# Kernel tuning notes

Hardware: AMD Instinct MI355X
Metric: run time of the kernel (lower is better)

## Reference

```python
import jax, jax.numpy as jnp
from jax import lax
import numpy as np

B, T, F = 256, 256, 40
H, A, HORIZON = 256, 64, 60
D_SP = 192


def setup_inputs() -> dict:
    key = jax.random.key(0)
    ks = jax.random.split(key, 16)
    s = 0.05  # weight scale to keep activations stable
    return {
        'x': jax.random.normal(ks[0], (B, T, F), jnp.float32),
        'W_sp': jax.random.normal(ks[1], (F, D_SP), jnp.float32) * s,
        'b_sp': jnp.zeros((D_SP,), jnp.float32),
        'Wx_ef': jax.random.normal(ks[2], (D_SP, 4 * H), jnp.float32) * s,
        'Wh_ef': jax.random.normal(ks[3], (H, 4 * H), jnp.float32) * s,
        'b_ef': jnp.zeros((4 * H,), jnp.float32),
        'Wx_eb': jax.random.normal(ks[4], (D_SP, 4 * H), jnp.float32) * s,
        'Wh_eb': jax.random.normal(ks[5], (H, 4 * H), jnp.float32) * s,
        'b_eb': jnp.zeros((4 * H,), jnp.float32),
        'We': jax.random.normal(ks[6], (2 * H, A), jnp.float32) * s,
        'Wd': jax.random.normal(ks[7], (H, A), jnp.float32) * s,
        'v': jax.random.normal(ks[8], (A,), jnp.float32) * s,
        'Wx_d': jax.random.normal(ks[9], (1 + 2 * H, 4 * H), jnp.float32) * s,
        'Wh_d': jax.random.normal(ks[10], (H, 4 * H), jnp.float32) * s,
        'b_d': jnp.zeros((4 * H,), jnp.float32),
        'W_ih': jax.random.normal(ks[11], (2 * H, H), jnp.float32) * s,
        'b_ih': jnp.zeros((H,), jnp.float32),
        'W_ic': jax.random.normal(ks[12], (2 * H, H), jnp.float32) * s,
        'b_ic': jnp.zeros((H,), jnp.float32),
        'Wo': jax.random.normal(ks[13], (H, 1), jnp.float32) * s,
        'bo': jnp.zeros((1,), jnp.float32),
    }


def _lstm_cell(x_t, h, c, Wx, Wh, b):
    g = x_t @ Wx + h @ Wh + b
    i, f, gg, o = jnp.split(g, 4, axis=-1)  # torch gate order i,f,g,o
    c = jax.nn.sigmoid(f) * c + jax.nn.sigmoid(i) * jnp.tanh(gg)
    h = jax.nn.sigmoid(o) * jnp.tanh(c)
    return h, c


def _lstm_scan(xs_tbd, Wx, Wh, b):
    # xs_tbd: [T, B, D] -> hs [T, B, H]
    h0 = jnp.zeros((xs_tbd.shape[1], Wh.shape[0]), xs_tbd.dtype)
    c0 = jnp.zeros_like(h0)
    def step(carry, x_t):
        h, c = carry
        h, c = _lstm_cell(x_t, h, c, Wx, Wh, b)
        return (h, c), h
    _, hs = lax.scan(step, (h0, c0), xs_tbd)
    return hs


def reference(x, W_sp, b_sp, Wx_ef, Wh_ef, b_ef, Wx_eb, Wh_eb, b_eb,
              We, Wd, v, Wx_d, Wh_d, b_d, W_ih, b_ih, W_ic, b_ic, Wo, bo):
    # spatial encoder (stand-in for DeepLOBEncoder): [B,T,F] -> [B,T,192]
    h_spatial = x @ W_sp + b_sp
    xs = jnp.swapaxes(h_spatial, 0, 1)          # [T, B, 192]
    hs_f = _lstm_scan(xs, Wx_ef, Wh_ef, b_ef)    # [T, B, H]
    hs_b = _lstm_scan(xs[::-1], Wx_eb, Wh_eb, b_eb)[::-1]
    enc_out = jnp.swapaxes(jnp.concatenate([hs_f, hs_b], axis=-1), 0, 1)  # [B,T,2H]

    enc_mean = enc_out.mean(axis=1)
    dec_h = jnp.tanh(enc_mean @ W_ih + b_ih)     # [B, H]
    dec_c = jnp.tanh(enc_mean @ W_ic + b_ic)

    enc_proj = enc_out @ We                      # [B, T, A] precomputed (same math)
    prev_y = ((x[:, -1, 0] + x[:, -1, 2]) / 2.0)[:, None]  # ask_idx=0, bid_idx=2

    def dec_step(carry, _):
        h, c, py = carry
        e = jnp.tanh(enc_proj + (h @ Wd)[:, None, :])        # [B,T,A]
        scores = e @ v                                        # [B,T]
        w = jax.nn.softmax(scores, axis=1)
        context = jnp.einsum('bt,bth->bh', w, enc_out)        # [B,2H]
        dec_in = jnp.concatenate([py, context], axis=1)       # [B,1+2H]
        h, c = _lstm_cell(dec_in, h, c, Wx_d, Wh_d, b_d)
        y = h @ Wo + bo                                       # [B,1]
        return (h, c, lax.stop_gradient(y)), y[:, 0]

    _, ys = lax.scan(dec_step, (dec_h, dec_c, prev_y), None, length=HORIZON)
    return jnp.swapaxes(ys, 0, 1)  # [B, horizon]
```

## Files before the change

kernel.cpp:

```cpp
#include <hip/hip_runtime.h>
#include <cmath>

#define B_ 256
#define T_ 256
#define F_ 40
#define H_ 256
#define A_ 64
#define HOR_ 60
#define DSP_ 192
#define ENC_NBLK 128
#define GRP_SZ 16
#define WSTR 456

typedef unsigned short u16;
typedef unsigned int u32;
typedef __attribute__((ext_vector_type(8))) short bf16x8;
typedef __attribute__((ext_vector_type(4))) float f32x4;
typedef __attribute__((ext_vector_type(8))) u32 u32x8;
typedef __attribute__((ext_vector_type(4))) u32 u32x4;

__device__ __forceinline__ float sigm(float x){ return 1.f/(1.f+expf(-x)); }

__device__ __forceinline__ u16 f2bf(float x){
  u32 u = __float_as_uint(x);
  u32 r = (u + 0x7FFFu + ((u>>16)&1u)) >> 16;
  return (u16)r;
}
__device__ __forceinline__ float bf2f(u16 h){ return __uint_as_float(((u32)h)<<16); }
__device__ __forceinline__ u32 packsplit(float x){
  u16 hi = f2bf(x);
  u16 lo = f2bf(x - bf2f(hi));
  return (u32)hi | ((u32)lo<<16);
}
__device__ __forceinline__ float unpack2f(u32 v){
  return __uint_as_float(v<<16) + __uint_as_float(v & 0xFFFF0000u);
}

__device__ __forceinline__ float wred_sum(float v){
  #pragma unroll
  for (int o=32;o>0;o>>=1) v += __shfl_xor(v,o);
  return v;
}
__device__ __forceinline__ float wred_max(float v){
  #pragma unroll
  for (int o=32;o>0;o>>=1) v = fmaxf(v,__shfl_xor(v,o));
  return v;
}

__global__ void conv_w(const float* __restrict__ Wx, const float* __restrict__ Wh,
                       u16* __restrict__ hi, u16* __restrict__ lo,
                       int KX, int Ktot, int N){
  int idx = blockIdx.x*256 + threadIdx.x;
  if (idx >= N*Ktot) return;
  int n = idx / Ktot, k = idx - n*Ktot;
  float w = (k < KX) ? Wx[(size_t)k*N + n] : Wh[(size_t)(k-KX)*N + n];
  u16 h = f2bf(w);
  hi[idx] = h;
  lo[idx] = f2bf(w - bf2f(h));
}

__global__ __launch_bounds__(192) void spatial_proj(
    const float* __restrict__ x, const float* __restrict__ W, const float* __restrict__ bsp,
    u32* __restrict__ hsp32){
  __shared__ float Ws[40][192];
  __shared__ float xr[40];
  int t = blockIdx.x, tid = threadIdx.x;
  for (int i = tid; i < 40*192; i += 192){ int k = i/192, c = i-k*192; Ws[k][c] = W[i]; }
  float bb = bsp[tid];
  __syncthreads();
  for (int b=0; b<B_; b++){
    if (tid < 40) xr[tid] = x[((size_t)b*T_ + t)*F_ + tid];
    __syncthreads();
    float acc = bb;
    #pragma unroll
    for (int k=0;k<40;k++) acc += xr[k]*Ws[k][tid];
    hsp32[((size_t)t*B_ + b)*DSP_ + tid] = packsplit(acc);
    __syncthreads();
  }
}

__global__ __launch_bounds__(256) void enc_scan(
    const u32* __restrict__ hsp32,
    const u16* __restrict__ W_hi, const u16* __restrict__ W_lo,
    const float* __restrict__ b_ef, const float* __restrict__ b_eb,
    u32* __restrict__ hbuf, u32* __restrict__ eo32, int* __restrict__ bar)
{
  extern __shared__ u16 smem[];
  u16* Whi = smem;
  u16* Wlo = smem + 4*16*WSTR;
  const int bid = blockIdx.x;
  const int grp = bid & 7;
  const int nt  = bid >> 3;
  const int dir = grp >> 2;
  const int m0  = (grp & 3) * 64;
  const int u0  = nt * 16;
  const int tid = threadIdx.x;
  const int wave = tid >> 6, lane = tid & 63;
  const int lrow = lane & 15, kblk = lane >> 4;
  const int koff = kblk * 8;
  {
    const size_t wbase = ((size_t)dir*1024 + u0) * 448;
    for (int idx = tid; idx < 4*16*448; idx += 256){
      int g = idx / (16*448);
      int r = idx - g*(16*448);
      int j = r / 448;
      int k = r - j*448;
      size_t go = wbase + ((size_t)g*256 + j)*448 + k;
      Whi[(g*16 + j)*WSTR + k] = W_hi[go];
      Wlo[(g*16 + j)*WSTR + k] = W_lo[go];
    }
  }
  const float* bias = dir ? b_eb : b_ef;
  float bg4[4];
  #pragma unroll
  for (int g=0; g<4; g++) bg4[g] = bias[g*H_ + u0 + lrow];
  __syncthreads();

  const int mrow = m0 + wave*16;
  const int arow = mrow + lrow;
  u32* hP0 = hbuf + (size_t)dir*(B_*H_);
  u32* hP1 = hbuf + (size_t)(2+dir)*(B_*H_);
  int* gbar = bar + grp*T_;
  float c_reg[4] = {0.f,0.f,0.f,0.f};

  for (int s=0; s<T_; s++){
    const int t = dir ? (T_-1-s) : s;
    f32x4 acc[4] = {};
    const u32* abase = hsp32 + ((size_t)t*B_ + arow)*DSP_;
    #pragma unroll
    for (int ks=0; ks<6; ks++){
      int kb = ks*32 + koff;
      u32x8 la = *(const u32x8*)(abase + kb);
      bf16x8 ah, al;
      #pragma unroll
      for (int j=0;j<8;j++){ ah[j]=(short)(la[j]&0xFFFFu); al[j]=(short)(la[j]>>16); }
      #pragma unroll
      for (int g=0; g<4; g++){
        bf16x8 bh = *(const bf16x8*)(Whi + (g*16+lrow)*WSTR + kb);
        bf16x8 bl = *(const bf16x8*)(Wlo + (g*16+lrow)*WSTR + kb);
        acc[g] = __builtin_amdgcn_mfma_f32_16x16x32_bf16(ah, bh, acc[g], 0,0,0);
        acc[g] = __builtin_amdgcn_mfma_f32_16x16x32_bf16(ah, bl, acc[g], 0,0,0);
        acc[g] = __builtin_amdgcn_mfma_f32_16x16x32_bf16(al, bh, acc[g], 0,0,0);
      }
    }
    if (s > 0){
      if (tid == 0){
        while (__hip_atomic_load(&gbar[s-1], __ATOMIC_ACQUIRE, __HIP_MEMORY_SCOPE_AGENT) < GRP_SZ)
          __builtin_amdgcn_s_sleep(1);
      }
      __syncthreads();
    }
    const u32* hin = (s & 1) ? hP1 : hP0;
    u32* hout      = (s & 1) ? hP0 : hP1;
    const u32* hbase = hin + (size_t)arow*H_;
    #pragma unroll
    for (int ks=0; ks<8; ks++){
      int kb = ks*32 + koff;
      u32x8 la = *(const u32x8*)(hbase + kb);
      bf16x8 ah, al;
      #pragma unroll
      for (int j=0;j<8;j++){ ah[j]=(short)(la[j]&0xFFFFu); al[j]=(short)(la[j]>>16); }
      #pragma unroll
      for (int g=0; g<4; g++){
        bf16x8 bh = *(const bf16x8*)(Whi + (g*16+lrow)*WSTR + 192 + kb);
        bf16x8 bl = *(const bf16x8*)(Wlo + (g*16+lrow)*WSTR + 192 + kb);
        acc[g] = __builtin_amdgcn_mfma_f32_16x16x32_bf16(ah, bh, acc[g], 0,0,0);
        acc[g] = __builtin_amdgcn_mfma_f32_16x16x32_bf16(ah, bl, acc[g], 0,0,0);
        acc[g] = __builtin_amdgcn_mfma_f32_16x16x32_bf16(al, bh, acc[g], 0,0,0);
      }
    }
    #pragma unroll
    for (int r=0; r<4; r++){
      int brow = mrow + kblk*4 + r;
      float gi = acc[0][r] + bg4[0];
      float gf = acc[1][r] + bg4[1];
      float gg = acc[2][r] + bg4[2];
      float go = acc[3][r] + bg4[3];
      float cn = sigm(gf)*c_reg[r] + sigm(gi)*tanhf(gg);
      float hn = sigm(go)*tanhf(cn);
      c_reg[r] = cn;
      u32 hp = packsplit(hn);
      hout[(size_t)brow*H_ + u0 + lrow] = hp;
      eo32[((size_t)brow*T_ + t)*512 + dir*H_ + u0 + lrow] = hp;
    }
    if (s == T_-1) break;
    __syncthreads();
    if (tid == 0)
      __hip_atomic_fetch_add(&gbar[s], 1, __ATOMIC_RELEASE, __HIP_MEMORY_SCOPE_AGENT);
  }
}

__global__ __launch_bounds__(512) void attn_step(
    const u32* __restrict__ eo32, const float* __restrict__ ep,
    const float* __restrict__ Wd, const float* __restrict__ v,
    const float* __restrict__ Wo, const float* __restrict__ bo,
    const float* __restrict__ h_dec, u32* __restrict__ Ad32,
    float* __restrict__ py, float* __restrict__ out, int s)
{
  __shared__ float sh_h[256], sh_hwd[64], sh_v[64], sh_sc[256], sh_w[256];
  __shared__ float red8[8][64];
  __shared__ float sh_red[4], sh_red2[4];
  __shared__ float redc[8][512];
  const int b = blockIdx.x, tid = threadIdx.x;
  const int wave = tid >> 6, lane = tid & 63;
  if (tid < 256) sh_h[tid] = h_dec[b*H_ + tid];
  if (tid >= 448) sh_v[tid-448] = v[tid-448];
  __syncthreads();
  if (s > 0) {
    if (tid < 256){
      float p = sh_h[tid] * Wo[tid];
      p = wred_sum(p);
      if ((tid & 63) == 0) sh_red[tid>>6] = p;
    }
    __syncthreads();
    if (tid == 0){
      float y = sh_red[0]+sh_red[1]+sh_red[2]+sh_red[3] + bo[0];
      out[b*HOR_ + (s-1)] = y;
      py[b] = y;
    }
  }
  {
    float ssum = 0.f;
    for (int j=wave*32; j<wave*32+32; j++) ssum += sh_h[j]*Wd[(size_t)j*A_ + lane];
    red8[wave][lane] = ssum;
    __syncthreads();
    if (tid < 64){
      float a = 0.f;
      #pragma unroll
      for (int q=0;q<8;q++) a += red8[q][tid];
      sh_hwd[tid] = a;
    }
  }
  __syncthreads();
  {
    int t = tid >> 1, aa = tid & 1;
    const float4* ep4 = (const float4*)(ep + ((size_t)(b*T_+t))*A_ + aa*32);
    float partial = 0.f;
    #pragma unroll
    for (int q=0;q<8;q++){
      float4 e4 = ep4[q];
      int a0 = aa*32 + q*4;
      partial += tanhf(e4.x + sh_hwd[a0+0]) * sh_v[a0+0];
      partial += tanhf(e4.y + sh_hwd[a0+1]) * sh_v[a0+1];
      partial += tanhf(e4.z + sh_hwd[a0+2]) * sh_v[a0+2];
      partial += tanhf(e4.w + sh_hwd[a0+3]) * sh_v[a0+3];
    }
    partial += __shfl_xor(partial, 1);
    if (aa == 0) sh_sc[t] = partial;
  }
  __syncthreads();
  if (tid < 256){
    float sc = sh_sc[tid];
    float m = wred_max(sc);
    if ((tid&63)==0) sh_red[tid>>6] = m;
    __syncthreads();
    m = fmaxf(fmaxf(sh_red[0],sh_red[1]), fmaxf(sh_red[2],sh_red[3]));
    float e = expf(sc - m);
    float su = wred_sum(e);
    if ((tid&63)==0) sh_red2[tid>>6] = su;
    __syncthreads();
    su = (sh_red2[0]+sh_red2[1])+(sh_red2[2]+sh_red2[3]);
    sh_w[tid] = e / su;
  } else { __syncthreads(); __syncthreads(); }
  __syncthreads();
  {
    float cacc[8] = {};
    const u32* eo = eo32 + (size_t)b*T_*512 + lane*8;
    #pragma unroll 8
    for (int tt=0; tt<32; tt++){
      int t = wave*32 + tt;
      float wgt = sh_w[t];
      u32x4 e0 = *(const u32x4*)(eo + (size_t)t*512);
      u32x4 e1 = *(const u32x4*)(eo + (size_t)t*512 + 4);
      #pragma unroll
      for (int j=0;j<4;j++){
        cacc[j]   += wgt * unpack2f(e0[j]);
        cacc[4+j] += wgt * unpack2f(e1[j]);
      }
    }
    #pragma unroll
    for (int j=0;j<8;j++) redc[wave][lane*8+j] = cacc[j];
  }
  __syncthreads();
  if (tid < 256){
    float c0 = 0.f, c1 = 0.f;
    #pragma unroll
    for (int q=0;q<8;q++){ c0 += redc[q][tid]; c1 += redc[q][256+tid]; }
    Ad32[(size_t)b*768 + tid]       = packsplit(c0);
    Ad32[(size_t)b*768 + 256 + tid] = packsplit(c1);
  }
}

__global__ __launch_bounds__(128) void dec_step_mfma(
    const u32* __restrict__ Ad32,
    const u16* __restrict__ W_hi, const u16* __restrict__ W_lo,
    const float* __restrict__ b_d, const float* __restrict__ Wx_d,
    const float* __restrict__ py,
    float* __restrict__ c_dec, float* __restrict__ h_dec,
    u32* __restrict__ AdW)
{
  const int u0 = blockIdx.x * 16;
  const int tid = threadIdx.x;
  const int wave = tid >> 6, lane = tid & 63;
  const int lrow = lane & 15, kblk = lane >> 4;
  const int u = u0 + lrow;
  const int mbase = blockIdx.y * 32 + wave * 16;
  const int koff = kblk * 8;
  size_t wro[4];
  #pragma unroll
  for (int g=0; g<4; g++) wro[g] = (size_t)(g*H_ + u) * 768;
  f32x4 acc[4] = {};
  const u32* abase = Ad32 + (size_t)(mbase + lrow)*768;
  for (int ks=0; ks<24; ks++){
    int kb = ks*32 + koff;
    u32x8 ld = *(const u32x8*)(abase + kb);
    bf16x8 ah, al;
    #pragma unroll
    for (int j=0;j<8;j++){ ah[j] = (short)(ld[j] & 0xFFFFu); al[j] = (short)(ld[j] >> 16); }
    #pragma unroll
    for (int g=0; g<4; g++){
      bf16x8 bh = *(const bf16x8*)(W_hi + wro[g] + kb);
      bf16x8 bl = *(const bf16x8*)(W_lo + wro[g] + kb);
      acc[g] = __builtin_amdgcn_mfma_f32_16x16x32_bf16(ah, bh, acc[g], 0,0,0);
      acc[g] = __builtin_amdgcn_mfma_f32_16x16x32_bf16(ah, bl, acc[g], 0,0,0);
      acc[g] = __builtin_amdgcn_mfma_f32_16x16x32_bf16(al, bh, acc[g], 0,0,0);
    }
  }
  float bg4[4], w0g[4];
  #pragma unroll
  for (int g=0;g<4;g++){ bg4[g] = b_d[g*H_ + u]; w0g[g] = Wx_d[g*H_ + u]; }
  #pragma unroll
  for (int r=0; r<4; r++){
    int bb = mbase + kblk*4 + r;
    float pyb = py[bb];
    float gi = acc[0][r] + bg4[0] + pyb*w0g[0];
    float gf = acc[1][r] + bg4[1] + pyb*w0g[1];
    float gg = acc[2][r] + bg4[2] + pyb*w0g[2];
    float go = acc[3][r] + bg4[3] + pyb*w0g[3];
    size_t ci = (size_t)bb*H_ + u;
    float cn = sigm(gf)*c_dec[ci] + sigm(gi)*tanhf(gg);
    float hn = sigm(go)*tanhf(cn);
    c_dec[ci] = cn;
    h_dec[ci] = hn;
    AdW[(size_t)bb*768 + 512 + u] = packsplit(hn);
  }
}

__global__ __launch_bounds__(256) void gemm_ep(
    const u32* __restrict__ eo32, const u16* __restrict__ Wet_hi, const u16* __restrict__ Wet_lo,
    float* __restrict__ ep)
{
  const int tid = threadIdx.x, wave = tid>>6, lane = tid&63;
  const int lrow = lane&15, kblk = lane>>4, koff = kblk*8;
  const size_t arow = (size_t)blockIdx.x*64 + wave*16 + lrow;
  f32x4 acc[4] = {};
  size_t wro[4];
  #pragma unroll
  for (int nf=0; nf<4; nf++) wro[nf] = (size_t)(nf*16 + lrow)*512;
  for (int ks=0; ks<16; ks++){
    int kb = ks*32 + koff;
    u32x8 ld = *(const u32x8*)(eo32 + arow*512 + kb);
    bf16x8 ah, al;
    #pragma unroll
    for (int j=0;j<8;j++){ ah[j] = (short)(ld[j] & 0xFFFFu); al[j] = (short)(ld[j] >> 16); }
    #pragma unroll
    for (int nf=0; nf<4; nf++){
      bf16x8 bh = *(const bf16x8*)(Wet_hi + wro[nf] + kb);
      bf16x8 bl = *(const bf16x8*)(Wet_lo + wro[nf] + kb);
      acc[nf] = __builtin_amdgcn_mfma_f32_16x16x32_bf16(ah, bh, acc[nf], 0,0,0);
      acc[nf] = __builtin_amdgcn_mfma_f32_16x16x32_bf16(ah, bl, acc[nf], 0,0,0);
      acc[nf] = __builtin_amdgcn_mfma_f32_16x16x32_bf16(al, bh, acc[nf], 0,0,0);
    }
  }
  #pragma unroll
  for (int nf=0; nf<4; nf++)
    #pragma unroll
    for (int r=0; r<4; r++){
      size_t orow = (size_t)blockIdx.x*64 + wave*16 + kblk*4 + r;
      ep[orow*64 + nf*16 + lrow] = acc[nf][r];
    }
}

__global__ __launch_bounds__(256) void sgemm_bias(
    const float* __restrict__ A, const float* __restrict__ W,
    const float* __restrict__ bias, float* __restrict__ C,
    int M, int N, int K, int act)
{
  __shared__ float As[64][17];
  __shared__ float Ws[16][64];
  int tid = threadIdx.x;
  int tr = tid >> 4, tc = tid & 15;
  int row0 = blockIdx.y * 64, col0 = blockIdx.x * 64;
  float acc[4][4] = {};
  for (int k0 = 0; k0 < K; k0 += 16) {
    for (int i = tid; i < 64*16; i += 256) {
      int r = i >> 4, kk = i & 15;
      int gr = row0 + r, gk = k0 + kk;
      As[r][kk] = (gr < M && gk < K) ? A[(size_t)gr*K + gk] : 0.f;
    }
    for (int i = tid; i < 16*64; i += 256) {
      int r = i >> 6, c = i & 63;
      int gk = k0 + r, gc = col0 + c;
      Ws[r][c] = (gk < K && gc < N) ? W[(size_t)gk*N + gc] : 0.f;
    }
    __syncthreads();
    #pragma unroll
    for (int kk=0;kk<16;kk++){
      float a0 = As[tr*4+0][kk], a1 = As[tr*4+1][kk];
      float a2v = As[tr*4+2][kk], a3 = As[tr*4+3][kk];
      float4 b4 = *(const float4*)&Ws[kk][tc*4];
      acc[0][0]+=a0*b4.x; acc[0][1]+=a0*b4.y; acc[0][2]+=a0*b4.z; acc[0][3]+=a0*b4.w;
      acc[1][0]+=a1*b4.x; acc[1][1]+=a1*b4.y; acc[1][2]+=a1*b4.z; acc[1][3]+=a1*b4.w;
      acc[2][0]+=a2v*b4.x; acc[2][1]+=a2v*b4.y; acc[2][2]+=a2v*b4.z; acc[2][3]+=a2v*b4.w;
      acc[3][0]+=a3*b4.x; acc[3][1]+=a3*b4.y; acc[3][2]+=a3*b4.z; acc[3][3]+=a3*b4.w;
    }
    __syncthreads();
  }
  #pragma unroll
  for (int i=0;i<4;i++){
    int r = row0 + tr*4 + i; if (r >= M) continue;
    #pragma unroll
    for (int j=0;j<4;j++){
      int c = col0 + tc*4 + j; if (c >= N) continue;
      float vv = acc[i][j] + (bias ? bias[c] : 0.f);
      if (act == 1) vv = tanhf(vv);
      C[(size_t)r*N + c] = vv;
    }
  }
}

__global__ __launch_bounds__(256) void final_y(const float* __restrict__ h_dec,
    const float* __restrict__ Wo, const float* __restrict__ bo, float* __restrict__ out){
  __shared__ float sh[4];
  int b = blockIdx.x, tid = threadIdx.x;
  float p = h_dec[b*H_+tid]*Wo[tid];
  p = wred_sum(p);
  if ((tid&63)==0) sh[tid>>6]=p;
  __syncthreads();
  if (tid==0) out[b*HOR_ + HOR_-1] = sh[0]+sh[1]+sh[2]+sh[3] + bo[0];
}

__global__ __launch_bounds__(256) void enc_mean_k(const u32* __restrict__ eo32,
                                                  float* __restrict__ em){
  __shared__ float redc[4][512];
  int b = blockIdx.x, tid = threadIdx.x;
  int wave = tid >> 6, lane = tid & 63;
  float cacc[8] = {};
  const u32* eo = eo32 + (size_t)b*T_*512 + lane*8;
  #pragma unroll 8
  for (int tt=0; tt<64; tt++){
    int t = wave*64 + tt;
    u32x4 e0 = *(const u32x4*)(eo + (size_t)t*512);
    u32x4 e1 = *(const u32x4*)(eo + (size_t)t*512 + 4);
    #pragma unroll
    for (int j=0;j<4;j++){ cacc[j] += unpack2f(e0[j]); cacc[4+j] += unpack2f(e1[j]); }
  }
  #pragma unroll
  for (int j=0;j<8;j++) redc[wave][lane*8+j] = cacc[j];
  __syncthreads();
  em[(size_t)b*512 + tid]       = (redc[0][tid]+redc[1][tid]+redc[2][tid]+redc[3][tid])*(1.f/T_);
  em[(size_t)b*512 + 256 + tid] = (redc[0][256+tid]+redc[1][256+tid]+redc[2][256+tid]+redc[3][256+tid])*(1.f/T_);
}

__global__ void pack_hd(const float* __restrict__ hd, u32* __restrict__ Ad32){
  int i = blockIdx.x*256 + threadIdx.x;
  int b = i >> 8, u = i & 255;
  Ad32[(size_t)b*768 + 512 + u] = packsplit(hd[i]);
}

__global__ void py_init(const float* __restrict__ x, float* __restrict__ py){
  int b = blockIdx.x*256 + threadIdx.x;
  if (b < B_)
    py[b] = (x[(size_t)b*T_*F_ + 255*F_ + 0] +
             x[(size_t)b*T_*F_ + 255*F_ + 2]) * 0.5f;
}

extern "C" void kernel_launch(void* const* d_in, const int* in_sizes, int n_in,
                              void* d_out, int out_size, void* d_ws, size_t ws_size,
                              hipStream_t stream)
{
  const float* x    = (const float*)d_in[0];
  const float* W_sp = (const float*)d_in[1];
  const float* b_sp = (const float*)d_in[2];
  const float* Wx_ef= (const float*)d_in[3];
  const float* Wh_ef= (const float*)d_in[4];
  const float* b_ef = (const float*)d_in[5];
  const float* Wx_eb= (const float*)d_in[6];
  const float* Wh_eb= (const float*)d_in[7];
  const float* b_eb = (const float*)d_in[8];
  const float* We   = (const float*)d_in[9];
  const float* Wd   = (const float*)d_in[10];
  const float* v    = (const float*)d_in[11];
  const float* Wx_d = (const float*)d_in[12];
  const float* Wh_d = (const float*)d_in[13];
  const float* b_d  = (const float*)d_in[14];
  const float* W_ih = (const float*)d_in[15];
  const float* b_ih = (const float*)d_in[16];
  const float* W_ic = (const float*)d_in[17];
  const float* b_ic = (const float*)d_in[18];
  const float* Wo   = (const float*)d_in[19];
  const float* bo   = (const float*)d_in[20];
  float* out = (float*)d_out;

  char* base = (char*)d_ws;
  auto alloc = [&](size_t bytes)->char*{
    char* p = base; base += (bytes + 255) & ~(size_t)255; return p;
  };
  u16* Wenc_hi = (u16*)alloc((size_t)2*1024*448*2);
  u16* Wenc_lo = (u16*)alloc((size_t)2*1024*448*2);
  u16* Wdec_hi = (u16*)alloc((size_t)1024*768*2);
  u16* Wdec_lo = (u16*)alloc((size_t)1024*768*2);
  u16* Wet_hi  = (u16*)alloc((size_t)64*512*2);
  u16* Wet_lo  = (u16*)alloc((size_t)64*512*2);
  u32* hsp32   = (u32*)alloc((size_t)T_*B_*DSP_*4);
  u32* hbuf    = (u32*)alloc((size_t)2*2*B_*H_*4);
  u32* eo32    = (u32*)alloc((size_t)B_*T_*512*4);
  float* em    = (float*)alloc((size_t)B_*512*4);
  float* ep    = (float*)alloc((size_t)B_*T_*64*4);
  float* hd    = (float*)alloc((size_t)B_*H_*4);
  float* cd    = (float*)alloc((size_t)B_*H_*4);
  u32* Ad32    = (u32*)alloc((size_t)B_*768*4);
  float* pyb   = (float*)alloc((size_t)B_*4);
  int* bar     = (int*)alloc((size_t)8*T_*4);
  if ((size_t)(base - (char*)d_ws) > ws_size) return;

  conv_w<<<dim3(1792),256,0,stream>>>(Wx_ef, Wh_ef, Wenc_hi, Wenc_lo, DSP_, 448, 1024);
  conv_w<<<dim3(1792),256,0,stream>>>(Wx_eb, Wh_eb, Wenc_hi+458752, Wenc_lo+458752, DSP_, 448, 1024);
  conv_w<<<dim3(3072),256,0,stream>>>(Wx_d+1024, Wh_d, Wdec_hi, Wdec_lo, 512, 768, 1024);
  conv_w<<<dim3(128),256,0,stream>>>(We, We, Wet_hi, Wet_lo, 512, 512, 64);

  spatial_proj<<<dim3(256),192,0,stream>>>(x, W_sp, b_sp, hsp32);

  hipMemsetAsync(hbuf, 0, (size_t)2*B_*H_*4, stream);
  hipMemsetAsync(bar, 0, (size_t)8*T_*4, stream);

  enc_scan<<<dim3(ENC_NBLK), dim3(256), 2*4*16*WSTR*2, stream>>>(
      hsp32, Wenc_hi, Wenc_lo, b_ef, b_eb, hbuf, eo32, bar);

  enc_mean_k<<<dim3(256),256,0,stream>>>(eo32, em);
  sgemm_bias<<<dim3(4,4),256,0,stream>>>(em, W_ih, b_ih, hd, B_, H_, 2*H_, 1);
  sgemm_bias<<<dim3(4,4),256,0,stream>>>(em, W_ic, b_ic, cd, B_, H_, 2*H_, 1);
  pack_hd<<<dim3(256),256,0,stream>>>(hd, Ad32);
  gemm_ep<<<dim3(1024),256,0,stream>>>(eo32, Wet_hi, Wet_lo, ep);
  py_init<<<dim3(1),256,0,stream>>>(x, pyb);

  for (int s=0; s<HOR_; s++){
    attn_step<<<dim3(256),512,0,stream>>>(eo32, ep, Wd, v, Wo, bo, hd, Ad32, pyb, out, s);
    dec_step_mfma<<<dim3(16,8),128,0,stream>>>(Ad32, Wdec_hi, Wdec_lo, b_d, Wx_d, pyb, cd, hd, Ad32);
  }
  final_y<<<dim3(256),256,0,stream>>>(hd, Wo, bo, out);
}
```

Baseline: 6.626 ms.

## Fuse decoder loop into persistent kernel with per-block flag synchronization

Replaces the 120 per-step decoder launches (attention plus LSTM cell) and the final output kernel with a single persistent kernel of 256 blocks. Blocks exchange data through padded per-block release/acquire flags in global memory instead of kernel boundaries, and the decoder hidden state is double-buffered. The encoder's counter barrier is switched to per-producer flags, and the signal is raised before the encoder-output store so that store overlaps the wait. This removes launch overhead and the implicit global syncs, at the cost of relying on all 256 blocks being co-resident and on spin-wait correctness.

New measurement: 5.920 ms. 10.7% less time.

```diff
diff --git a/kernel.cpp b/kernel.cpp
--- a/kernel.cpp
+++ b/kernel.cpp
@@ -11,6 +11,8 @@
 #define ENC_NBLK 128
 #define GRP_SZ 16
 #define WSTR 456
+#define FPAD 32
+#define ADLD 1024
 
 typedef unsigned short u16;
 typedef unsigned int u32;
@@ -45,6 +47,18 @@
   #pragma unroll
   for (int o=32;o>0;o>>=1) v = fmaxf(v,__shfl_xor(v,o));
   return v;
+}
+
+__device__ __forceinline__ void flags_signal(int* f){
+  __hip_atomic_store(f, 1, __ATOMIC_RELEASE, __HIP_MEMORY_SCOPE_AGENT);
+}
+__device__ __forceinline__ void flags_wait(const int* base, int n, int wave, int lane){
+  if (wave == 0 && lane < n){
+    const int* f = base + (size_t)lane*FPAD;
+    while (__hip_atomic_load(f, __ATOMIC_ACQUIRE, __HIP_MEMORY_SCOPE_AGENT) == 0)
+      __builtin_amdgcn_s_sleep(1);
+  }
+  __syncthreads();
 }
 
 __global__ void conv_w(const float* __restrict__ Wx, const float* __restrict__ Wh,
@@ -83,7 +97,7 @@
     const u32* __restrict__ hsp32,
     const u16* __restrict__ W_hi, const u16* __restrict__ W_lo,
     const float* __restrict__ b_ef, const float* __restrict__ b_eb,
-    u32* __restrict__ hbuf, u32* __restrict__ eo32, int* __restrict__ bar)
+    u32* __restrict__ hbuf, u32* __restrict__ eo32, int* __restrict__ ebar)
 {
   extern __shared__ u16 smem[];
   u16* Whi = smem;
@@ -120,7 +134,6 @@
   const int arow = mrow + lrow;
   u32* hP0 = hbuf + (size_t)dir*(B_*H_);
   u32* hP1 = hbuf + (size_t)(2+dir)*(B_*H_);
-  int* gbar = bar + grp*T_;
   float c_reg[4] = {0.f,0.f,0.f,0.f};
 
   for (int s=0; s<T_; s++){
@@ -143,13 +156,8 @@
         acc[g] = __builtin_amdgcn_mfma_f32_16x16x32_bf16(al, bh, acc[g], 0,0,0);
       }
     }
-    if (s > 0){
-      if (tid == 0){
-        while (__hip_atomic_load(&gbar[s-1], __ATOMIC_ACQUIRE, __HIP_MEMORY_SCOPE_AGENT) < GRP_SZ)
-          __builtin_amdgcn_s_sleep(1);
-      }
-      __syncthreads();
-    }
+    if (s > 0)
+      flags_wait(ebar + (size_t)((grp*T_ + (s-1))*16)*FPAD, GRP_SZ, wave, lane);
     const u32* hin = (s & 1) ? hP1 : hP0;
     u32* hout      = (s & 1) ? hP0 : hP1;
     const u32* hbase = hin + (size_t)arow*H_;
@@ -169,9 +177,9 @@
         acc[g] = __builtin_amdgcn_mfma_f32_16x16x32_bf16(al, bh, acc[g], 0,0,0);
       }
     }
+    u32 hp4[4];
     #pragma unroll
     for (int r=0; r<4; r++){
-      int brow = mrow + kblk*4 + r;
       float gi = acc[0][r] + bg4[0];
       float gf = acc[1][r] + bg4[1];
       float gg = acc[2][r] + bg4[2];
@@ -179,170 +187,183 @@
       float cn = sigm(gf)*c_reg[r] + sigm(gi)*tanhf(gg);
       float hn = sigm(go)*tanhf(cn);
       c_reg[r] = cn;
-      u32 hp = packsplit(hn);
-      hout[(size_t)brow*H_ + u0 + lrow] = hp;
-      eo32[((size_t)brow*T_ + t)*512 + dir*H_ + u0 + lrow] = hp;
-    }
-    if (s == T_-1) break;
-    __syncthreads();
-    if (tid == 0)
-      __hip_atomic_fetch_add(&gbar[s], 1, __ATOMIC_RELEASE, __HIP_MEMORY_SCOPE_AGENT);
-  }
-}
-
-__global__ __launch_bounds__(512) void attn_step(
+      hp4[r] = packsplit(hn);
+      hout[(size_t)(mrow + kblk*4 + r)*H_ + u0 + lrow] = hp4[r];
+    }
+    __syncthreads();
+    if (s < T_-1 && tid == 0)
+      flags_signal(ebar + (size_t)((grp*T_ + s)*16 + nt)*FPAD);
+    #pragma unroll
+    for (int r=0; r<4; r++)
+      eo32[((size_t)(mrow + kblk*4 + r)*T_ + t)*512 + dir*H_ + u0 + lrow] = hp4[r];
+  }
+}
+
+__global__ __launch_bounds__(512) void dec_scan(
     const u32* __restrict__ eo32, const float* __restrict__ ep,
     const float* __restrict__ Wd, const float* __restrict__ v,
     const float* __restrict__ Wo, const float* __restrict__ bo,
-    const float* __restrict__ h_dec, u32* __restrict__ Ad32,
-    float* __restrict__ py, float* __restrict__ out, int s)
+    const u16* __restrict__ W_hi, const u16* __restrict__ W_lo,
+    const float* __restrict__ b_d, const float* __restrict__ Wx_d,
+    float* __restrict__ hdp, const float* __restrict__ cd0,
+    u32* __restrict__ Ad32, float* __restrict__ py,
+    float* __restrict__ out, int* __restrict__ fA, int* __restrict__ fB)
 {
   __shared__ float sh_h[256], sh_hwd[64], sh_v[64], sh_sc[256], sh_w[256];
   __shared__ float red8[8][64];
   __shared__ float sh_red[4], sh_red2[4];
   __shared__ float redc[8][512];
+  __shared__ float gl[4][16][16];
   const int b = blockIdx.x, tid = threadIdx.x;
   const int wave = tid >> 6, lane = tid & 63;
-  if (tid < 256) sh_h[tid] = h_dec[b*H_ + tid];
-  if (tid >= 448) sh_v[tid-448] = v[tid-448];
-  __syncthreads();
-  if (s > 0) {
+  const int bx = b & 15, by = b >> 4;
+  const int cr = tid >> 4, cu = tid & 15;
+  float c_reg = 0.f;
+  float bg0=0,bg1=0,bg2=0,bg3=0, w00=0,w01=0,w02=0,w03=0;
+  if (tid < 256){
+    c_reg = cd0[(size_t)(by*16+cr)*H_ + bx*16+cu];
+    int uu = bx*16 + cu;
+    bg0 = b_d[uu];       bg1 = b_d[256+uu];
+    bg2 = b_d[512+uu];   bg3 = b_d[768+uu];
+    w00 = Wx_d[uu];      w01 = Wx_d[256+uu];
+    w02 = Wx_d[512+uu];  w03 = Wx_d[768+uu];
+  }
+  for (int s=0; s<=HOR_; s++){
+    if (s > 0)
+      flags_wait(fB + (size_t)(((s-1)*16 + (b>>4))*16)*FPAD, 16, wave, lane);
+    const float* hsrc = hdp + (size_t)(s&1)*B_*H_;
+    if (tid < 256) sh_h[tid] = hsrc[(size_t)b*H_ + tid];
+    if (tid >= 448) sh_v[tid-448] = v[tid-448];
+    __syncthreads();
+    if (s > 0){
+      if (tid < 256){
+        float p = sh_h[tid] * Wo[tid];
+        p = wred_sum(p);
+        if ((tid & 63) == 0) sh_red[tid>>6] = p;
+      }
+      __syncthreads();
+      if (tid == 0){
+        float y = sh_red[0]+sh_red[1]+sh_red[2]+sh_red[3] + bo[0];
+        out[b*HOR_ + (s-1)] = y;
+        py[b] = y;
+      }
+    }
+    if (s == HOR_) break;
+    {
+      float ssum = 0.f;
+      for (int j=wave*32; j<wave*32+32; j++) ssum += sh_h[j]*Wd[(size_t)j*A_ + lane];
+      red8[wave][lane] = ssum;
+      __syncthreads();
+      if (tid < 64){
+        float a = 0.f;
+        #pragma unroll
+        for (int q=0;q<8;q++) a += red8[q][tid];
+        sh_hwd[tid] = a;
+      }
+    }
+    __syncthreads();
+    {
+      int t = tid >> 1, aa = tid & 1;
+      const float4* ep4 = (const float4*)(ep + ((size_t)(b*T_+t))*A_ + aa*32);
+      float partial = 0.f;
+      #pragma unroll
+      for (int q=0;q<8;q++){
+        float4 e4 = ep4[q];
+        int a0 = aa*32 + q*4;
+        partial += tanhf(e4.x + sh_hwd[a0+0]) * sh_v[a0+0];
+        partial += tanhf(e4.y + sh_hwd[a0+1]) * sh_v[a0+1];
+        partial += tanhf(e4.z + sh_hwd[a0+2]) * sh_v[a0+2];
+        partial += tanhf(e4.w + sh_hwd[a0+3]) * sh_v[a0+3];
+      }
+      partial += __shfl_xor(partial, 1);
+      if (aa == 0) sh_sc[t] = partial;
+    }
+    __syncthreads();
     if (tid < 256){
-      float p = sh_h[tid] * Wo[tid];
-      p = wred_sum(p);
-      if ((tid & 63) == 0) sh_red[tid>>6] = p;
-    }
-    __syncthreads();
-    if (tid == 0){
-      float y = sh_red[0]+sh_red[1]+sh_red[2]+sh_red[3] + bo[0];
-      out[b*HOR_ + (s-1)] = y;
-      py[b] = y;
-    }
-  }
-  {
-    float ssum = 0.f;
-    for (int j=wave*32; j<wave*32+32; j++) ssum += sh_h[j]*Wd[(size_t)j*A_ + lane];
-    red8[wave][lane] = ssum;
-    __syncthreads();
-    if (tid < 64){
-      float a = 0.f;
-      #pragma unroll
-      for (int q=0;q<8;q++) a += red8[q][tid];
-      sh_hwd[tid] = a;
-    }
-  }
-  __syncthreads();
-  {
-    int t = tid >> 1, aa = tid & 1;
-    const float4* ep4 = (const float4*)(ep + ((size_t)(b*T_+t))*A_ + aa*32);
-    float partial = 0.f;
-    #pragma unroll
-    for (int q=0;q<8;q++){
-      float4 e4 = ep4[q];
-      int a0 = aa*32 + q*4;
-      partial += tanhf(e4.x + sh_hwd[a0+0]) * sh_v[a0+0];
-      partial += tanhf(e4.y + sh_hwd[a0+1]) * sh_v[a0+1];
-      partial += tanhf(e4.z + sh_hwd[a0+2]) * sh_v[a0+2];
-      partial += tanhf(e4.w + sh_hwd[a0+3]) * sh_v[a0+3];
-    }
-    partial += __shfl_xor(partial, 1);
-    if (aa == 0) sh_sc[t] = partial;
-  }
-  __syncthreads();
-  if (tid < 256){
-    float sc = sh_sc[tid];
-    float m = wred_max(sc);
-    if ((tid&63)==0) sh_red[tid>>6] = m;
-    __syncthreads();
-    m = fmaxf(fmaxf(sh_red[0],sh_red[1]), fmaxf(sh_red[2],sh_red[3]));
-    float e = expf(sc - m);
-    float su = wred_sum(e);
-    if ((tid&63)==0) sh_red2[tid>>6] = su;
-    __syncthreads();
-    su = (sh_red2[0]+sh_red2[1])+(sh_red2[2]+sh_red2[3]);
-    sh_w[tid] = e / su;
-  } else { __syncthreads(); __syncthreads(); }
-  __syncthreads();
-  {
-    float cacc[8] = {};
-    const u32* eo = eo32 + (size_t)b*T_*512 + lane*8;
-    #pragma unroll 8
-    for (int tt=0; tt<32; tt++){
-      int t = wave*32 + tt;
-      float wgt = sh_w[t];
-      u32x4 e0 = *(const u32x4*)(eo + (size_t)t*512);
-      u32x4 e1 = *(const u32x4*)(eo + (size_t)t*512 + 4);
-      #pragma unroll
-      for (int j=0;j<4;j++){
-        cacc[j]   += wgt * unpack2f(e0[j]);
-        cacc[4+j] += wgt * unpack2f(e1[j]);
-      }
-    }
-    #pragma unroll
-    for (int j=0;j<8;j++) redc[wave][lane*8+j] = cacc[j];
-  }
-  __syncthreads();
-  if (tid < 256){
-    float c0 = 0.f, c1 = 0.f;
-    #pragma unroll
-    for (int q=0;q<8;q++){ c0 += redc[q][tid]; c1 += redc[q][256+tid]; }
-    Ad32[(size_t)b*768 + tid]       = packsplit(c0);
-    Ad32[(size_t)b*768 + 256 + tid] = packsplit(c1);
-  }
-}
-
-__global__ __launch_bounds__(128) void dec_step_mfma(
-    const u32* __restrict__ Ad32,
-    const u16* __restrict__ W_hi, const u16* __restrict__ W_lo,
-    const float* __restrict__ b_d, const float* __restrict__ Wx_d,
-    const float* __restrict__ py,
-    float* __restrict__ c_dec, float* __restrict__ h_dec,
-    u32* __restrict__ AdW)
-{
-  const int u0 = blockIdx.x * 16;
-  const int tid = threadIdx.x;
-  const int wave = tid >> 6, lane = tid & 63;
-  const int lrow = lane & 15, kblk = lane >> 4;
-  const int u = u0 + lrow;
-  const int mbase = blockIdx.y * 32 + wave * 16;
-  const int koff = kblk * 8;
-  size_t wro[4];
-  #pragma unroll
-  for (int g=0; g<4; g++) wro[g] = (size_t)(g*H_ + u) * 768;
-  f32x4 acc[4] = {};
-  const u32* abase = Ad32 + (size_t)(mbase + lrow)*768;
-  for (int ks=0; ks<24; ks++){
-    int kb = ks*32 + koff;
-    u32x8 ld = *(const u32x8*)(abase + kb);
-    bf16x8 ah, al;
-    #pragma unroll
-    for (int j=0;j<8;j++){ ah[j] = (short)(ld[j] & 0xFFFFu); al[j] = (short)(ld[j] >> 16); }
-    #pragma unroll
-    for (int g=0; g<4; g++){
-      bf16x8 bh = *(const bf16x8*)(W_hi + wro[g] + kb);
-      bf16x8 bl = *(const bf16x8*)(W_lo + wro[g] + kb);
-      acc[g] = __builtin_amdgcn_mfma_f32_16x16x32_bf16(ah, bh, acc[g], 0,0,0);
-      acc[g] = __builtin_amdgcn_mfma_f32_16x16x32_bf16(ah, bl, acc[g], 0,0,0);
-      acc[g] = __builtin_amdgcn_mfma_f32_16x16x32_bf16(al, bh, acc[g], 0,0,0);
-    }
-  }
-  float bg4[4], w0g[4];
-  #pragma unroll
-  for (int g=0;g<4;g++){ bg4[g] = b_d[g*H_ + u]; w0g[g] = Wx_d[g*H_ + u]; }
-  #pragma unroll
-  for (int r=0; r<4; r++){
-    int bb = mbase + kblk*4 + r;
-    float pyb = py[bb];
-    float gi = acc[0][r] + bg4[0] + pyb*w0g[0];
-    float gf = acc[1][r] + bg4[1] + pyb*w0g[1];
-    float gg = acc[2][r] + bg4[2] + pyb*w0g[2];
-    float go = acc[3][r] + bg4[3] + pyb*w0g[3];
-    size_t ci = (size_t)bb*H_ + u;
-    float cn = sigm(gf)*c_dec[ci] + sigm(gi)*tanhf(gg);
-    float hn = sigm(go)*tanhf(cn);
-    c_dec[ci] = cn;
-    h_dec[ci] = hn;
-    AdW[(size_t)bb*768 + 512 + u] = packsplit(hn);
+      float sc = sh_sc[tid];
+      float m = wred_max(sc);
+      if ((tid&63)==0) sh_red[tid>>6] = m;
+      __syncthreads();
+      m = fmaxf(fmaxf(sh_red[0],sh_red[1]), fmaxf(sh_red[2],sh_red[3]));
+      float e = expf(sc - m);
+      float su = wred_sum(e);
+      if ((tid&63)==0) sh_red2[tid>>6] = su;
+      __syncthreads();
+      su = (sh_red2[0]+sh_red2[1])+(sh_red2[2]+sh_red2[3]);
+      sh_w[tid] = e / su;
+    } else { __syncthreads(); __syncthreads(); }
+    __syncthreads();
+    {
+      float cacc[8] = {};
+      const u32* eo = eo32 + (size_t)b*T_*512 + lane*8;
+      #pragma unroll 8
+      for (int tt=0; tt<32; tt++){
+        int t = wave*32 + tt;
+        float wgt = sh_w[t];
+        u32x4 e0 = *(const u32x4*)(eo + (size_t)t*512);
+        u32x4 e1 = *(const u32x4*)(eo + (size_t)t*512 + 4);
+        #pragma unroll
+        for (int j=0;j<4;j++){
+          cacc[j]   += wgt * unpack2f(e0[j]);
+          cacc[4+j] += wgt * unpack2f(e1[j]);
+        }
+      }
+      #pragma unroll
+      for (int j=0;j<8;j++) redc[wave][lane*8+j] = cacc[j];
+    }
+    __syncthreads();
+    if (tid < 256){
+      float c0 = 0.f, c1 = 0.f;
+      #pragma unroll
+      for (int q=0;q<8;q++){ c0 += redc[q][tid]; c1 += redc[q][256+tid]; }
+      Ad32[(size_t)b*ADLD + tid]       = packsplit(c0);
+      Ad32[(size_t)b*ADLD + 256 + tid] = packsplit(c1);
+    }
+    __syncthreads();
+    if (tid == 0)
+      flags_signal(fA + (size_t)((s*16 + (b>>4))*16 + (b&15))*FPAD);
+    flags_wait(fA + (size_t)((s*16 + by)*16)*FPAD, 16, wave, lane);
+    const int par = s & 1;
+    if (wave < 4){
+      const int g = wave;
+      const int r16 = lane & 15, kb4 = lane >> 4;
+      f32x4 acc = {0.f,0.f,0.f,0.f};
+      const u32* ar = Ad32 + (size_t)(by*16 + r16)*ADLD;
+      const u16* WH = W_hi + (size_t)(g*256 + bx*16 + r16)*768;
+      const u16* WL = W_lo + (size_t)(g*256 + bx*16 + r16)*768;
+      for (int ks=0; ks<24; ks++){
+        int kb = ks*32 + kb4*8;
+        int kp = (kb < 512) ? kb : (kb + (par<<8));
+        u32x8 ld = *(const u32x8*)(ar + kp);
+        bf16x8 ah, al;
+        #pragma unroll
+        for (int j=0;j<8;j++){ ah[j]=(short)(ld[j]&0xFFFFu); al[j]=(short)(ld[j]>>16); }
+        bf16x8 bh = *(const bf16x8*)(WH + kb);
+        bf16x8 bl = *(const bf16x8*)(WL + kb);
+        acc = __builtin_amdgcn_mfma_f32_16x16x32_bf16(ah, bh, acc, 0,0,0);
+        acc = __builtin_amdgcn_mfma_f32_16x16x32_bf16(ah, bl, acc, 0,0,0);
+        acc = __builtin_amdgcn_mfma_f32_16x16x32_bf16(al, bh, acc, 0,0,0);
+      }
+      #pragma unroll
+      for (int vv=0; vv<4; vv++) gl[g][kb4*4+vv][r16] = acc[vv];
+    }
+    __syncthreads();
+    if (tid < 256){
+      float pyr = py[by*16 + cr];
+      float gi = gl[0][cr][cu] + bg0 + pyr*w00;
+      float gf = gl[1][cr][cu] + bg1 + pyr*w01;
+      float gg = gl[2][cr][cu] + bg2 + pyr*w02;
+      float go = gl[3][cr][cu] + bg3 + pyr*w03;
+      float cn = sigm(gf)*c_reg + sigm(gi)*tanhf(gg);
+      float hn = sigm(go)*tanhf(cn);
+      c_reg = cn;
+      size_t ridx = (size_t)(by*16+cr)*H_ + bx*16+cu;
+      hdp[(size_t)((s+1)&1)*B_*H_ + ridx] = hn;
+      Ad32[(size_t)(by*16+cr)*ADLD + 512 + (((s+1)&1)<<8) + bx*16+cu] = packsplit(hn);
+    }
+    __syncthreads();
+    if (tid == 0)
+      flags_signal(fB + (size_t)((s*16 + by)*16 + bx)*FPAD);
   }
 }
 
@@ -429,17 +450,6 @@
   }
 }
 
-__global__ __launch_bounds__(256) void final_y(const float* __restrict__ h_dec,
-    const float* __restrict__ Wo, const float* __restrict__ bo, float* __restrict__ out){
-  __shared__ float sh[4];
-  int b = blockIdx.x, tid = threadIdx.x;
-  float p = h_dec[b*H_+tid]*Wo[tid];
-  p = wred_sum(p);
-  if ((tid&63)==0) sh[tid>>6]=p;
-  __syncthreads();
-  if (tid==0) out[b*HOR_ + HOR_-1] = sh[0]+sh[1]+sh[2]+sh[3] + bo[0];
-}
-
 __global__ __launch_bounds__(256) void enc_mean_k(const u32* __restrict__ eo32,
                                                   float* __restrict__ em){
   __shared__ float redc[4][512];
@@ -462,10 +472,13 @@
   em[(size_t)b*512 + 256 + tid] = (redc[0][256+tid]+redc[1][256+tid]+redc[2][256+tid]+redc[3][256+tid])*(1.f/T_);
 }
 
-__global__ void pack_hd(const float* __restrict__ hd, u32* __restrict__ Ad32){
+__global__ void pack_hd(const float* __restrict__ hd, u32* __restrict__ Ad32,
+                        float* __restrict__ hdp){
   int i = blockIdx.x*256 + threadIdx.x;
   int b = i >> 8, u = i & 255;
-  Ad32[(size_t)b*768 + 512 + u] = packsplit(hd[i]);
+  float h0 = hd[i];
+  hdp[i] = h0;
+  Ad32[(size_t)b*ADLD + 512 + u] = packsplit(h0);
 }
 
 __global__ void py_init(const float* __restrict__ x, float* __restrict__ py){
@@ -519,9 +532,12 @@
   float* ep    = (float*)alloc((size_t)B_*T_*64*4);
   float* hd    = (float*)alloc((size_t)B_*H_*4);
   float* cd    = (float*)alloc((size_t)B_*H_*4);
-  u32* Ad32    = (u32*)alloc((size_t)B_*768*4);
+  float* hdp   = (float*)alloc((size_t)2*B_*H_*4);
+  u32* Ad32    = (u32*)alloc((size_t)B_*ADLD*4);
   float* pyb   = (float*)alloc((size_t)B_*4);
-  int* bar     = (int*)alloc((size_t)8*T_*4);
+  int* ebar    = (int*)alloc((size_t)8*T_*16*FPAD*4);
+  int* fA      = (int*)alloc((size_t)HOR_*16*16*FPAD*4);
+  int* fB      = (int*)alloc((size_t)HOR_*16*16*FPAD*4);
   if ((size_t)(base - (char*)d_ws) > ws_size) return;
 
   conv_w<<<dim3(1792),256,0,stream>>>(Wx_ef, Wh_ef, Wenc_hi, Wenc_lo, DSP_, 448, 1024);
@@ -532,21 +548,21 @@
   spatial_proj<<<dim3(256),192,0,stream>>>(x, W_sp, b_sp, hsp32);
 
   hipMemsetAsync(hbuf, 0, (size_t)2*B_*H_*4, stream);
-  hipMemsetAsync(bar, 0, (size_t)8*T_*4, stream);
+  hipMemsetAsync(ebar, 0, (size_t)8*T_*16*FPAD*4, stream);
+  hipMemsetAsync(fA, 0, (size_t)HOR_*16*16*FPAD*4, stream);
+  hipMemsetAsync(fB, 0, (size_t)HOR_*16*16*FPAD*4, stream);
 
   enc_scan<<<dim3(ENC_NBLK), dim3(256), 2*4*16*WSTR*2, stream>>>(
-      hsp32, Wenc_hi, Wenc_lo, b_ef, b_eb, hbuf, eo32, bar);
+      hsp32, Wenc_hi, Wenc_lo, b_ef, b_eb, hbuf, eo32, ebar);
 
   enc_mean_k<<<dim3(256),256,0,stream>>>(eo32, em);
   sgemm_bias<<<dim3(4,4),256,0,stream>>>(em, W_ih, b_ih, hd, B_, H_, 2*H_, 1);
   sgemm_bias<<<dim3(4,4),256,0,stream>>>(em, W_ic, b_ic, cd, B_, H_, 2*H_, 1);
-  pack_hd<<<dim3(256),256,0,stream>>>(hd, Ad32);
+  pack_hd<<<dim3(256),256,0,stream>>>(hd, Ad32, hdp);
   gemm_ep<<<dim3(1024),256,0,stream>>>(eo32, Wet_hi, Wet_lo, ep);
   py_init<<<dim3(1),256,0,stream>>>(x, pyb);
 
-  for (int s=0; s<HOR_; s++){
-    attn_step<<<dim3(256),512,0,stream>>>(eo32, ep, Wd, v, Wo, bo, hd, Ad32, pyb, out, s);
-    dec_step_mfma<<<dim3(16,8),128,0,stream>>>(Ad32, Wdec_hi, Wdec_lo, b_d, Wx_d, pyb, cd, hd, Ad32);
-  }
-  final_y<<<dim3(256),256,0,stream>>>(hd, Wo, bo, out);
-}
+  dec_scan<<<dim3(256),512,0,stream>>>(
+      eo32, ep, Wd, v, Wo, bo, Wdec_hi, Wdec_lo, b_d, Wx_d,
+      hdp, cd, Ad32, pyb, out, fA, fB);
+}
```
